# Optimization experiments

Measured on AMD Instinct MI355X. Metric: run time of the kernel, lower is better.

## Reference

```python
import jax, jax.numpy as jnp
import numpy as np

B, N, E = 2, 20000, 200000
IN_F, OUT_F, HEADS = 256, 32, 4
NEG_SLOPE = 0.2


def setup_inputs() -> dict:
    key = jax.random.key(0)
    k1, k2, k3, k4 = jax.random.split(key, 4)
    x = jax.random.normal(k1, (B, N, IN_F), dtype=jnp.float32)
    edge_indices = jax.random.randint(k2, (2, E), 0, N, dtype=jnp.int64)
    # xavier-uniform-like scales
    W = jax.random.normal(k3, (OUT_F * HEADS, IN_F), dtype=jnp.float32) * np.float32(1.0 / np.sqrt(IN_F))
    a = jax.random.normal(k4, (2 * OUT_F, 1), dtype=jnp.float32) * np.float32(0.1)
    return {"x": x, "edge_indices": edge_indices, "W": W, "a": a}


def reference(x, edge_indices, W, a):
    Bq, Nq, _ = x.shape
    Hh, Ff = HEADS, OUT_F
    # h: [B, N, H, F]
    h = (x @ W.T).reshape(Bq, Nq, Hh, Ff)
    src, dst = edge_indices[0], edge_indices[1]
    Eq = src.shape[0]
    h_src = h[:, src]  # [B, E, H, F]
    h_dst = h[:, dst]  # [B, E, H, F]
    # scores = leaky_relu(concat(h_src, h_dst) @ a)  without materializing concat
    a_src, a_dst = a[:Ff, 0], a[Ff:, 0]
    scores = (jnp.einsum('behf,f->beh', h_src, a_src)
              + jnp.einsum('behf,f->beh', h_dst, a_dst))
    scores = jnp.where(scores > 0, scores, NEG_SLOPE * scores)  # LeakyReLU(0.2)
    # Original applies softmax over dim=0 (the BATCH dim) per edge
    sm = jax.nn.softmax(scores, axis=0)  # [B, E, H]
    # Original loop overwrites attention_weights[:, src] per edge, so only the
    # LAST edge with a given src survives.
    edge_ids = jnp.arange(Eq, dtype=jnp.int32)
    last_edge = jax.ops.segment_max(edge_ids, src, num_segments=Nq)
    has_edge = jax.ops.segment_sum(jnp.ones((Eq,), jnp.int32), src, num_segments=Nq) > 0
    last_edge = jnp.clip(last_edge, 0, Eq - 1)
    aw = jnp.where(has_edge[None, :, None], sm[:, last_edge], 0.0)  # [B, N, H]
    # aggregated[:, s] = aw[:, s] * sum_{edges i: src[i]==s} h_dst[:, i]
    seg = jax.ops.segment_sum(jnp.transpose(h_dst, (1, 0, 2, 3)), src, num_segments=Nq)  # [N,B,H,F]
    seg = jnp.transpose(seg, (1, 0, 2, 3))  # [B, N, H, F]
    aggregated = aw[..., None] * seg
    # mean over heads; dropout is identity in eval mode
    return aggregated.mean(axis=2)  # [B, N, F]
```

## Files before the change

kernel.cpp:

```cpp
#include <hip/hip_runtime.h>
#include <hip/hip_bf16.h>

#define BB 2
#define NN 20000
#define EE 200000
#define INF 256
#define OUTF 32
#define NH 4
#define HF 128
#define NEG_SLOPE 0.2f
#define GEMM_BLOCKS 1250
#define EDGE_BLOCKS 98
#define CAP 96
#define OVF_CAP 8192

using bf16 = __hip_bfloat16;
typedef __attribute__((ext_vector_type(8))) short bf16x8;
typedef __attribute__((ext_vector_type(4))) float f32x4;

__device__ __forceinline__ float bf2f(unsigned short s){ return __uint_as_float((unsigned)s << 16); }
__device__ __forceinline__ ushort f2bf_bits(float f){
    __hip_bfloat16 b = __float2bfloat16(f);
    return *(ushort*)&b;
}

__device__ __forceinline__ int get_src(const int* ei, int e, int f64){
    return f64 ? ei[2 * e] : ei[e];
}
__device__ __forceinline__ int get_dst(const int* ei, int e, int f64){
    return f64 ? ei[2 * EE + 2 * e] : ei[EE + e];
}

__global__ void k_init(const ushort* __restrict__ xr, const int* __restrict__ er,
                       const void* __restrict__ Wv,
                       int* __restrict__ flags, ushort* __restrict__ wbf,
                       int* __restrict__ cnt, int* __restrict__ last_e,
                       int* __restrict__ ovf_cnt){
    int i = blockIdx.x * blockDim.x + threadIdx.x;
    if (i < NN){ cnt[i] = 0; last_e[i] = -1; }
    if (i == 0) *ovf_cnt = 0;
    if (blockIdx.x == 0){
        __shared__ int cnt_big, cnt_nz;
        if (threadIdx.x == 0){ cnt_big = 0; cnt_nz = 0; }
        __syncthreads();
        int big = 0;
        for (int k = threadIdx.x; k < 8192; k += blockDim.x){
            unsigned e = ((unsigned)xr[2 * k] >> 7) & 0xff;
            if (e >= 0xC0) big++;
        }
        int nz = 0;
        for (int k = threadIdx.x; k < 4096; k += blockDim.x){
            if (er[2 * k + 1] != 0) nz++;
        }
        atomicAdd(&cnt_big, big);
        atomicAdd(&cnt_nz, nz);
        __syncthreads();
        if (threadIdx.x == 0){
            flags[0] = (cnt_big >= 16) ? 1 : 0;
            flags[1] = (cnt_nz == 0) ? 1 : 0;
        }
        const bool f32w = (cnt_big >= 16);
        for (int fr = threadIdx.x; fr < 4096; fr += blockDim.x){
            int lane = fr & 63;
            int t    = (fr >> 6) & 3;
            int kc   = (fr >> 8) & 7;
            int ch   = fr >> 11;
            int col  = ch * 64 + t * 16 + (lane & 15);
            int kb   = kc * 32 + (lane >> 4) * 8;
            bf16x8 v;
            if (f32w){
                const float* wg = (const float*)Wv + (size_t)col * INF + kb;
                #pragma unroll
                for (int j = 0; j < 8; ++j) v[j] = (short)f2bf_bits(wg[j]);
            } else {
                const ushort* wg = (const ushort*)Wv + (size_t)col * INF + kb;
                #pragma unroll
                for (int j = 0; j < 8; ++j) v[j] = (short)wg[j];
            }
            *(bf16x8*)(wbf + (size_t)fr * 8) = v;
        }
    }
}

__global__ __launch_bounds__(256, 4)
void k_gemm(const void* __restrict__ xv_, const ushort* __restrict__ wbf,
            const void* __restrict__ av, const int* __restrict__ ei,
            const int* __restrict__ flags, ushort* __restrict__ h,
            float* __restrict__ alpha_s, float* __restrict__ alpha_d,
            int* __restrict__ last_e, int* __restrict__ cnt,
            ushort* __restrict__ slots, int* __restrict__ ovf_cnt,
            int* __restrict__ ovf_list){
    if (blockIdx.x >= GEMM_BLOCKS){
        int f64 = flags[1];
        int t = (blockIdx.x - GEMM_BLOCKS) * 256 + threadIdx.x;
        for (int e = t; e < EE; e += EDGE_BLOCKS * 256){
            int s = get_src(ei, e, f64);
            int d = get_dst(ei, e, f64);
            atomicMax(&last_e[s], e);
            int idx = atomicAdd(&cnt[s], 1);
            if (idx < CAP) slots[(size_t)s * CAP + idx] = (ushort)d;
            else { int o = atomicAdd(ovf_cnt, 1); if (o < OVF_CAP) ovf_list[o] = e; }
        }
        return;
    }

    const int tid  = threadIdx.x;
    const int lane = tid & 63;
    const int w    = tid >> 6;
    const int l15  = lane & 15;
    const int q    = lane >> 4;
    const bool f32 = flags[0] != 0;

    const int row0 = blockIdx.x * 32 + (w >> 1) * 16;
    const int ch   = w & 1;
    const int hd0  = ch * 2;

    f32x4 acc[4];
    #pragma unroll
    for (int t = 0; t < 4; ++t) acc[t] = (f32x4){0.f, 0.f, 0.f, 0.f};

    const ushort* wb = wbf + (size_t)ch * 16384;

    if (f32){
        const float* xp = (const float*)xv_ + (size_t)(row0 + l15) * INF + q * 8;
        float4 raw[8][2];
        #pragma unroll
        for (int kc = 0; kc < 8; ++kc){
            const float4* p = (const float4*)(xp + kc * 32);
            raw[kc][0] = p[0];
            raw[kc][1] = p[1];
        }
        #pragma unroll
        for (int kc = 0; kc < 8; ++kc){
            float4 lo = raw[kc][0], hi = raw[kc][1];
            bf16x8 afrag;
            afrag[0] = (short)f2bf_bits(lo.x); afrag[1] = (short)f2bf_bits(lo.y);
            afrag[2] = (short)f2bf_bits(lo.z); afrag[3] = (short)f2bf_bits(lo.w);
            afrag[4] = (short)f2bf_bits(hi.x); afrag[5] = (short)f2bf_bits(hi.y);
            afrag[6] = (short)f2bf_bits(hi.z); afrag[7] = (short)f2bf_bits(hi.w);
            #pragma unroll
            for (int t = 0; t < 4; ++t){
                bf16x8 bfrag = *(const bf16x8*)(wb + (((size_t)kc * 4 + t) * 64 + lane) * 8);
                acc[t] = __builtin_amdgcn_mfma_f32_16x16x32_bf16(afrag, bfrag, acc[t], 0, 0, 0);
            }
        }
    } else {
        const ushort* xp = (const ushort*)xv_ + (size_t)(row0 + l15) * INF + q * 8;
        #pragma unroll
        for (int kc = 0; kc < 8; ++kc){
            bf16x8 afrag = *(const bf16x8*)(xp + kc * 32);
            #pragma unroll
            for (int t = 0; t < 4; ++t){
                bf16x8 bfrag = *(const bf16x8*)(wb + (((size_t)kc * 4 + t) * 64 + lane) * 8);
                acc[t] = __builtin_amdgcn_mfma_f32_16x16x32_bf16(afrag, bfrag, acc[t], 0, 0, 0);
            }
        }
    }

    #pragma unroll
    for (int r = 0; r < 4; ++r){
        int row = row0 + q * 4 + r;
        #pragma unroll
        for (int t = 0; t < 2; ++t){
            unsigned v = (unsigned)f2bf_bits(acc[t][r])
                       | ((unsigned)f2bf_bits(acc[t + 2][r]) << 16);
            int f = t * 16 + l15;
            *(unsigned*)(h + (size_t)row * HF + f * 4 + hd0) = v;
        }
    }

    float as_lo, as_hi, ad_lo, ad_hi;
    if (f32){
        const float* af = (const float*)av;
        as_lo = af[l15];        as_hi = af[16 + l15];
        ad_lo = af[OUTF + l15]; ad_hi = af[OUTF + 16 + l15];
    } else {
        const ushort* ab = (const ushort*)av;
        as_lo = bf2f(ab[l15]);        as_hi = bf2f(ab[16 + l15]);
        ad_lo = bf2f(ab[OUTF + l15]); ad_hi = bf2f(ab[OUTF + 16 + l15]);
    }
    #pragma unroll
    for (int r = 0; r < 4; ++r){
        int row = row0 + q * 4 + r;
        #pragma unroll
        for (int hp = 0; hp < 2; ++hp){
            int t0 = hp * 2, t1 = hp * 2 + 1;
            float ps = acc[t0][r] * as_lo + acc[t1][r] * as_hi;
            float pd = acc[t0][r] * ad_lo + acc[t1][r] * ad_hi;
            ps += __shfl_down(ps, 8, 16); pd += __shfl_down(pd, 8, 16);
            ps += __shfl_down(ps, 4, 16); pd += __shfl_down(pd, 4, 16);
            ps += __shfl_down(ps, 2, 16); pd += __shfl_down(pd, 2, 16);
            ps += __shfl_down(ps, 1, 16); pd += __shfl_down(pd, 1, 16);
            if (l15 == 0){
                size_t o = (size_t)row * NH + hd0 + hp;
                alpha_s[o] = ps;
                alpha_d[o] = pd;
            }
        }
    }
}

__global__ void k_aw(const int* __restrict__ ei, const int* __restrict__ flags,
                     const int* __restrict__ last_e,
                     const float* __restrict__ alpha_s, const float* __restrict__ alpha_d,
                     float* __restrict__ aw){
    int n = blockIdx.x * blockDim.x + threadIdx.x;
    if (n >= NN) return;
    int le = last_e[n];
    if (le < 0){
        #pragma unroll
        for (int hh = 0; hh < NH; ++hh){
            aw[((size_t)0 * NN + n) * NH + hh] = 0.f;
            aw[((size_t)1 * NN + n) * NH + hh] = 0.f;
        }
        return;
    }
    int d = get_dst(ei, le, flags[1]);
    #pragma unroll
    for (int hh = 0; hh < NH; ++hh){
        float s0 = alpha_s[((size_t)0 * NN + n) * NH + hh] + alpha_d[((size_t)0 * NN + d) * NH + hh];
        float s1 = alpha_s[((size_t)1 * NN + n) * NH + hh] + alpha_d[((size_t)1 * NN + d) * NH + hh];
        s0 = s0 > 0.f ? s0 : NEG_SLOPE * s0;
        s1 = s1 > 0.f ? s1 : NEG_SLOPE * s1;
        float m  = fmaxf(s0, s1);
        float e0 = __expf(s0 - m);
        float e1 = __expf(s1 - m);
        float inv = 1.f / (e0 + e1);
        aw[((size_t)0 * NN + n) * NH + hh] = 0.25f * e0 * inv;
        aw[((size_t)1 * NN + n) * NH + hh] = 0.25f * e1 * inv;
    }
}

__global__ __launch_bounds__(256)
void k_agg(const ushort* __restrict__ slots, const int* __restrict__ cnt,
           const ushort* __restrict__ h, const float* __restrict__ aw,
           float* __restrict__ out_f){
    int lane = threadIdx.x & 63;
    int wid  = (blockIdx.x * blockDim.x + threadIdx.x) >> 6;
    int nw   = (gridDim.x * blockDim.x) >> 6;
    int b = lane >> 5;
    int f = lane & 31;
    for (int n = wid; n < NN; n += nw){
        int m = cnt[n]; if (m > CAP) m = CAP;
        const ushort* sl = slots + (size_t)n * CAP;
        const ushort* hb = h + (size_t)b * NN * HF + f * 4;
        float ax = 0.f, ay = 0.f, az = 0.f, aww = 0.f;
        int i = 0;
        for (; i + 4 <= m; i += 4){
            ushort4 dd = *(const ushort4*)(sl + i);
            ushort4 u0 = *(const ushort4*)(hb + (size_t)dd.x * HF);
            ushort4 u1 = *(const ushort4*)(hb + (size_t)dd.y * HF);
            ushort4 u2 = *(const ushort4*)(hb + (size_t)dd.z * HF);
            ushort4 u3 = *(const ushort4*)(hb + (size_t)dd.w * HF);
            ax += bf2f(u0.x) + bf2f(u1.x) + bf2f(u2.x) + bf2f(u3.x);
            ay += bf2f(u0.y) + bf2f(u1.y) + bf2f(u2.y) + bf2f(u3.y);
            az += bf2f(u0.z) + bf2f(u1.z) + bf2f(u2.z) + bf2f(u3.z);
            aww += bf2f(u0.w) + bf2f(u1.w) + bf2f(u2.w) + bf2f(u3.w);
        }
        for (; i < m; ++i){
            ushort4 u = *(const ushort4*)(hb + (size_t)sl[i] * HF);
            ax += bf2f(u.x); ay += bf2f(u.y); az += bf2f(u.z); aww += bf2f(u.w);
        }
        float4 awv = *(const float4*)(aw + ((size_t)b * NN + n) * NH);
        out_f[((size_t)b * NN + n) * OUTF + f] =
            awv.x * ax + awv.y * ay + awv.z * az + awv.w * aww;
    }
}

__global__ void k_fix(const int* __restrict__ ei, const int* __restrict__ flags,
                      const int* __restrict__ ovf_cnt, const int* __restrict__ ovf_list,
                      const ushort* __restrict__ h, const float* __restrict__ aw,
                      float* __restrict__ out_f){
    int lane = threadIdx.x & 63;
    int wid  = (blockIdx.x * blockDim.x + threadIdx.x) >> 6;
    int nw   = (gridDim.x * blockDim.x) >> 6;
    int b = lane >> 5;
    int f = lane & 31;
    int M = *ovf_cnt; if (M > OVF_CAP) M = OVF_CAP;
    int f64 = flags[1];
    for (int i = wid; i < M; i += nw){
        int e = ovf_list[i];
        int s = get_src(ei, e, f64);
        int d = get_dst(ei, e, f64);
        float4 awv = *(const float4*)(aw + ((size_t)b * NN + s) * NH);
        ushort4 u = *(const ushort4*)(h + ((size_t)b * NN + d) * HF + f * 4);
        float acc = awv.x * bf2f(u.x) + awv.y * bf2f(u.y)
                  + awv.z * bf2f(u.z) + awv.w * bf2f(u.w);
        atomicAdd(&out_f[((size_t)b * NN + s) * OUTF + f], acc);
    }
}

extern "C" void kernel_launch(void* const* d_in, const int* in_sizes, int n_in,
                              void* d_out, int out_size, void* d_ws, size_t ws_size,
                              hipStream_t stream){
    const void* x = d_in[0]; const void* eiv = d_in[1];
    const void* W = d_in[2]; const void* a  = d_in[3];
    for (int i = 0; i < n_in; ++i){
        if      (in_sizes[i] == BB * NN * INF) x   = d_in[i];
        else if (in_sizes[i] == 2 * EE)        eiv = d_in[i];
        else if (in_sizes[i] == HF * INF)      W   = d_in[i];
        else if (in_sizes[i] == 2 * OUTF)      a   = d_in[i];
    }
    const int* ei = (const int*)eiv;
    float* out = (float*)d_out;

    const size_t HN = (size_t)BB * NN * HF;
    char* p = (char*)d_ws;
    int*    flags    = (int*)p;                       p += 64;
    ushort* wbf      = (ushort*)p;                    p += 32768 * 2;
    ushort* h        = (ushort*)p;                    p += HN * 2;
    float*  alpha_s  = (float*)p;                     p += (size_t)BB * NN * NH * 4;
    float*  alpha_d  = (float*)p;                     p += (size_t)BB * NN * NH * 4;
    float*  aw       = (float*)p;                     p += (size_t)BB * NN * NH * 4;
    int*    last_e   = (int*)p;                       p += (size_t)NN * 4;
    int*    cnt      = (int*)p;                       p += (size_t)NN * 4;
    int*    ovf_cnt  = (int*)p;                       p += 64;
    int*    ovf_list = (int*)p;                       p += (size_t)OVF_CAP * 4;
    ushort* slots    = (ushort*)p;

    k_init <<<(NN + 255) / 256, 256, 0, stream>>>((const ushort*)x, ei, W, flags, wbf,
                                                  cnt, last_e, ovf_cnt);
    k_gemm <<<GEMM_BLOCKS + EDGE_BLOCKS, 256, 0, stream>>>(x, wbf, a, ei, flags, h,
                                                           alpha_s, alpha_d, last_e,
                                                           cnt, slots, ovf_cnt, ovf_list);
    k_aw   <<<(NN + 255) / 256, 256, 0, stream>>>(ei, flags, last_e, alpha_s, alpha_d, aw);
    k_agg  <<<2048, 256, 0, stream>>>(slots, cnt, h, aw, out);
    k_fix  <<<32, 256, 0, stream>>>(ei, flags, ovf_cnt, ovf_list, h, aw, out);
}
```

Before: 157.7 us.

## Stage x and W tiles in LDS with per-block head-chunk split

Remaps the GEMM blocks so each block computes 64 rows for a single head-chunk, where before each block computed 32 rows across both chunks. Each block first stages its W chunk and an XOR-swizzled bf16 copy of its x tile in shared memory, then feeds the MFMAs from LDS. The goal is to replace repeated per-wave global W fragment loads with shared-memory reuse. In exchange, x is now read by two blocks, every block (including the edge-binning blocks) allocates 64KB of LDS, and occupancy is lowered.

Measured after the change: 165.1 us. +4.7%, slower.

```diff
diff --git a/kernel.cpp b/kernel.cpp
--- a/kernel.cpp
+++ b/kernel.cpp
@@ -82,7 +82,7 @@
     }
 }
 
-__global__ __launch_bounds__(256, 4)
+__global__ __launch_bounds__(256, 2)
 void k_gemm(const void* __restrict__ xv_, const ushort* __restrict__ wbf,
             const void* __restrict__ av, const int* __restrict__ ei,
             const int* __restrict__ flags, ushort* __restrict__ h,
@@ -90,6 +90,9 @@
             int* __restrict__ last_e, int* __restrict__ cnt,
             ushort* __restrict__ slots, int* __restrict__ ovf_cnt,
             int* __restrict__ ovf_list){
+    __shared__ ushort lx[64 * 256];
+    __shared__ ushort lw[16384];
+
     if (blockIdx.x >= GEMM_BLOCKS){
         int f64 = flags[1];
         int t = (blockIdx.x - GEMM_BLOCKS) * 256 + threadIdx.x;
@@ -111,52 +114,65 @@
     const int q    = lane >> 4;
     const bool f32 = flags[0] != 0;
 
-    const int row0 = blockIdx.x * 32 + (w >> 1) * 16;
-    const int ch   = w & 1;
-    const int hd0  = ch * 2;
+    const int rb      = blockIdx.x >> 1;
+    const int ch      = blockIdx.x & 1;
+    const int hd0     = ch * 2;
+    const int row_blk = rb * 64;
+
+    {
+        const ushort* wsrc = wbf + (size_t)ch * 16384;
+        #pragma unroll
+        for (int i = 0; i < 8; ++i){
+            int off = tid * 8 + i * 2048;
+            *(bf16x8*)&lw[off] = *(const bf16x8*)(wsrc + off);
+        }
+    }
+    {
+        int r = tid >> 2, kbase = (tid & 3) * 64;
+        if (f32){
+            const float* xg = (const float*)xv_ + (size_t)(row_blk + r) * INF + kbase;
+            #pragma unroll
+            for (int jj = 0; jj < 8; ++jj){
+                float4 a = *(const float4*)(xg + jj * 8);
+                float4 b = *(const float4*)(xg + jj * 8 + 4);
+                bf16x8 v;
+                v[0] = (short)f2bf_bits(a.x); v[1] = (short)f2bf_bits(a.y);
+                v[2] = (short)f2bf_bits(a.z); v[3] = (short)f2bf_bits(a.w);
+                v[4] = (short)f2bf_bits(b.x); v[5] = (short)f2bf_bits(b.y);
+                v[6] = (short)f2bf_bits(b.z); v[7] = (short)f2bf_bits(b.w);
+                int kphys = (kbase + jj * 8 + 8 * r) & 255;
+                *(bf16x8*)&lx[r * 256 + kphys] = v;
+            }
+        } else {
+            const ushort* xg = (const ushort*)xv_ + (size_t)(row_blk + r) * INF + kbase;
+            #pragma unroll
+            for (int jj = 0; jj < 8; ++jj){
+                bf16x8 v = *(const bf16x8*)(xg + jj * 8);
+                int kphys = (kbase + jj * 8 + 8 * r) & 255;
+                *(bf16x8*)&lx[r * 256 + kphys] = v;
+            }
+        }
+    }
+    __syncthreads();
 
     f32x4 acc[4];
     #pragma unroll
     for (int t = 0; t < 4; ++t) acc[t] = (f32x4){0.f, 0.f, 0.f, 0.f};
 
-    const ushort* wb = wbf + (size_t)ch * 16384;
-
-    if (f32){
-        const float* xp = (const float*)xv_ + (size_t)(row0 + l15) * INF + q * 8;
-        float4 raw[8][2];
-        #pragma unroll
-        for (int kc = 0; kc < 8; ++kc){
-            const float4* p = (const float4*)(xp + kc * 32);
-            raw[kc][0] = p[0];
-            raw[kc][1] = p[1];
-        }
-        #pragma unroll
-        for (int kc = 0; kc < 8; ++kc){
-            float4 lo = raw[kc][0], hi = raw[kc][1];
-            bf16x8 afrag;
-            afrag[0] = (short)f2bf_bits(lo.x); afrag[1] = (short)f2bf_bits(lo.y);
-            afrag[2] = (short)f2bf_bits(lo.z); afrag[3] = (short)f2bf_bits(lo.w);
-            afrag[4] = (short)f2bf_bits(hi.x); afrag[5] = (short)f2bf_bits(hi.y);
-            afrag[6] = (short)f2bf_bits(hi.z); afrag[7] = (short)f2bf_bits(hi.w);
-            #pragma unroll
-            for (int t = 0; t < 4; ++t){
-                bf16x8 bfrag = *(const bf16x8*)(wb + (((size_t)kc * 4 + t) * 64 + lane) * 8);
-                acc[t] = __builtin_amdgcn_mfma_f32_16x16x32_bf16(afrag, bfrag, acc[t], 0, 0, 0);
-            }
-        }
-    } else {
-        const ushort* xp = (const ushort*)xv_ + (size_t)(row0 + l15) * INF + q * 8;
-        #pragma unroll
-        for (int kc = 0; kc < 8; ++kc){
-            bf16x8 afrag = *(const bf16x8*)(xp + kc * 32);
-            #pragma unroll
-            for (int t = 0; t < 4; ++t){
-                bf16x8 bfrag = *(const bf16x8*)(wb + (((size_t)kc * 4 + t) * 64 + lane) * 8);
-                acc[t] = __builtin_amdgcn_mfma_f32_16x16x32_bf16(afrag, bfrag, acc[t], 0, 0, 0);
-            }
-        }
-    }
-
+    const int rr = w * 16 + l15;
+    #pragma unroll
+    for (int kc = 0; kc < 8; ++kc){
+        int k0 = kc * 32 + q * 8;
+        int kphys = (k0 + 8 * rr) & 255;
+        bf16x8 afrag = *(const bf16x8*)&lx[rr * 256 + kphys];
+        #pragma unroll
+        for (int t = 0; t < 4; ++t){
+            bf16x8 bfrag = *(const bf16x8*)&lw[(((size_t)kc * 4 + t) * 64 + lane) * 8];
+            acc[t] = __builtin_amdgcn_mfma_f32_16x16x32_bf16(afrag, bfrag, acc[t], 0, 0, 0);
+        }
+    }
+
+    const int row0 = row_blk + w * 16;
     #pragma unroll
     for (int r = 0; r < 4; ++r){
         int row = row0 + q * 4 + r;
```
